# Optimization experiments

Hardware: AMD Instinct MI355X
Metric: run time of the kernel (lower is better)

The kernel has to match this reference:

```python
import jax, jax.numpy as jnp
import numpy as np

B, S, FEAT, H, DK, MAX_ITEMS = 8, 1024, 512, 8, 64, 200
LN_EPS = 1e-5
NEG = -999999999.0


def _build_mask(seq_len):
    # rows before T = S-(maxItems+1) cannot see the tail block [T:];
    # tail rows T..S-2 cannot see columns >= their own index (strict upper wedge).
    T = seq_len - (MAX_ITEMS + 1)
    i = jnp.arange(seq_len)[:, None]
    j = jnp.arange(seq_len)[None, :]
    blocked = ((i < T) & (j >= T)) | ((i >= T) & (i <= seq_len - 2) & (j >= i))
    return jnp.where(blocked, NEG, 0.0).astype(jnp.float32)  # [S, S]


def setup_inputs() -> dict:
    key = jax.random.key(0)
    ks = jax.random.split(key, 6)
    def init(k, shape, fan_in):
        return (jax.random.normal(k, shape, jnp.float32) / np.sqrt(fan_in)).astype(jnp.float32)
    return {
        "x": jax.random.normal(ks[0], (B, S, FEAT), jnp.float32),
        "ln_gamma": jnp.ones((FEAT,), jnp.float32),
        "ln_beta": jnp.zeros((FEAT,), jnp.float32),
        "WQ": init(ks[1], (H, FEAT, DK), FEAT), "bq": jnp.zeros((H, DK), jnp.float32),
        "WK": init(ks[2], (H, FEAT, DK), FEAT), "bk": jnp.zeros((H, DK), jnp.float32),
        "WV": init(ks[3], (H, FEAT, DK), FEAT), "bv": jnp.zeros((H, DK), jnp.float32),
        "WO": init(ks[4], (H * DK, FEAT), H * DK), "bO": jnp.zeros((FEAT,), jnp.float32),
    }


def reference(x, ln_gamma, ln_beta, WQ, bq, WK, bk, WV, bv, WO, bO):
    b, s, f = x.shape
    # Pre-LN
    mu = jnp.mean(x, axis=-1, keepdims=True)
    var = jnp.mean((x - mu) ** 2, axis=-1, keepdims=True)
    xn = (x - mu) / jnp.sqrt(var + LN_EPS) * ln_gamma + ln_beta
    # per-head projections, heads stacked: [B, H, S, DK]
    q = jnp.einsum('bsf,hfd->bhsd', xn, WQ) + bq[None, :, None, :]
    k = jnp.einsum('bsf,hfd->bhsd', xn, WK) + bk[None, :, None, :]
    v = jnp.einsum('bsf,hfd->bhsd', xn, WV) + bv[None, :, None, :]
    scores = jnp.einsum('bhsd,bhtd->bhst', q, k) / np.sqrt(DK).astype(np.float32)
    scores = scores + _build_mask(s)[None, None, :, :]
    attn = jax.nn.softmax(scores, axis=-1)
    z = jnp.einsum('bhst,bhtd->bhsd', attn, v)           # [B, H, S, DK]
    z = jnp.transpose(z, (0, 2, 1, 3)).reshape(b, s, -1)  # concat heads -> [B, S, H*DK]
    return z @ WO + bO
```

## Files before the change

kernel.cpp:

```cpp
#include <hip/hip_runtime.h>

typedef __bf16 bf16;
typedef __attribute__((ext_vector_type(8))) __bf16 bf16x8;
typedef __attribute__((ext_vector_type(4))) __bf16 bf16x4;
typedef __attribute__((ext_vector_type(4))) float f32x4;

#define QSCL 0.18033688011112042f
#define RESCALE_THR 8.0f

#if __has_builtin(__builtin_amdgcn_exp2f)
#define EXP2(x) __builtin_amdgcn_exp2f(x)
#else
#define EXP2(x) exp2f(x)
#endif

__device__ __forceinline__ void gload16(const void* g, void* l) {
  __builtin_amdgcn_global_load_lds(
      (const __attribute__((address_space(1))) void*)g,
      (__attribute__((address_space(3))) void*)l, 16, 0, 0);
}

__global__ void pack_kernel(const float* __restrict__ WQ, const float* __restrict__ WK,
                            const float* __restrict__ WV, const float* __restrict__ WO,
                            bf16* __restrict__ Bt, bf16* __restrict__ WOt) {
  int idx = blockIdx.x * 256 + threadIdx.x;
  if (idx < 1536 * 512) {
    int n = idx >> 9, k = idx & 511;
    int mat = n >> 9, rem = n & 511, h = rem >> 6, d = rem & 63;
    const float* W = (mat == 0) ? WQ : ((mat == 1) ? WK : WV);
    Bt[idx] = (bf16)W[((size_t)h * 512 + k) * 64 + d];
  } else {
    int j = idx - 1536 * 512;
    int n = j >> 9, k = j & 511;
    WOt[j] = (bf16)WO[(size_t)k * 512 + n];
  }
}

__global__ void ln_kernel(const float* __restrict__ x, const float* __restrict__ gam,
                          const float* __restrict__ bet, bf16* __restrict__ xn) {
  int wave = threadIdx.x >> 6, lane = threadIdx.x & 63;
  int row = blockIdx.x * 4 + wave;
  const float4* xr = (const float4*)(x + (size_t)row * 512);
  float4 v0 = xr[lane], v1 = xr[lane + 64];
  float s  = v0.x + v0.y + v0.z + v0.w + v1.x + v1.y + v1.z + v1.w;
  float s2 = v0.x * v0.x + v0.y * v0.y + v0.z * v0.z + v0.w * v0.w
           + v1.x * v1.x + v1.y * v1.y + v1.z * v1.z + v1.w * v1.w;
  #pragma unroll
  for (int m = 1; m < 64; m <<= 1) { s += __shfl_xor(s, m); s2 += __shfl_xor(s2, m); }
  float mu = s * (1.f / 512.f);
  float rstd = rsqrtf(s2 * (1.f / 512.f) - mu * mu + 1e-5f);
  const float4* gr = (const float4*)gam;
  const float4* br = (const float4*)bet;
  float4 g0 = gr[lane], g1 = gr[lane + 64], b0 = br[lane], b1 = br[lane + 64];
  bf16x4 o0, o1;
  o0[0] = (bf16)((v0.x - mu) * rstd * g0.x + b0.x);
  o0[1] = (bf16)((v0.y - mu) * rstd * g0.y + b0.y);
  o0[2] = (bf16)((v0.z - mu) * rstd * g0.z + b0.z);
  o0[3] = (bf16)((v0.w - mu) * rstd * g0.w + b0.w);
  o1[0] = (bf16)((v1.x - mu) * rstd * g1.x + b1.x);
  o1[1] = (bf16)((v1.y - mu) * rstd * g1.y + b1.y);
  o1[2] = (bf16)((v1.z - mu) * rstd * g1.z + b1.z);
  o1[3] = (bf16)((v1.w - mu) * rstd * g1.w + b1.w);
  *(bf16x4*)(xn + (size_t)row * 512 + lane * 4) = o0;
  *(bf16x4*)(xn + (size_t)row * 512 + 256 + lane * 4) = o1;
}

template <int MODE>
__global__ __launch_bounds__(256) void gemm_kernel(
    const bf16* __restrict__ A, const bf16* __restrict__ Bt, float* __restrict__ outF,
    bf16* __restrict__ qb, bf16* __restrict__ kb, bf16* __restrict__ vtb,
    const float* __restrict__ biasQ, const float* __restrict__ biasK,
    const float* __restrict__ biasV, const float* __restrict__ biasO) {
  __shared__ bf16 sA[128 * 32];
  __shared__ bf16 sB[128 * 32];
  const int tid = threadIdx.x;
  const int wave = tid >> 6, lane = tid & 63;
  const int m0 = blockIdx.x * 128, n0 = blockIdx.y * 128;
  const int wm = (wave >> 1) * 64, wn = (wave & 1) * 64;
  const int lrow = lane & 15, lk = (lane >> 4) * 8;
  const int srow = lane >> 2, scol = (lane & 3) * 8;
  f32x4 acc[4][4] = {};
  for (int kt = 0; kt < 512; kt += 32) {
    __syncthreads();
    #pragma unroll
    for (int c = 0; c < 2; ++c) {
      const int ch = wave * 2 + c;
      gload16(A + (size_t)(m0 + ch * 16 + srow) * 512 + kt + scol, &sA[ch * 512]);
      gload16(Bt + (size_t)(n0 + ch * 16 + srow) * 512 + kt + scol, &sB[ch * 512]);
    }
    __syncthreads();
    bf16x8 af[4], bfr[4];
    #pragma unroll
    for (int mi = 0; mi < 4; ++mi)
      af[mi] = *(const bf16x8*)&sA[(wm + mi * 16 + lrow) * 32 + lk];
    #pragma unroll
    for (int ni = 0; ni < 4; ++ni)
      bfr[ni] = *(const bf16x8*)&sB[(wn + ni * 16 + lrow) * 32 + lk];
    #pragma unroll
    for (int mi = 0; mi < 4; ++mi)
      #pragma unroll
      for (int ni = 0; ni < 4; ++ni)
        acc[mi][ni] = __builtin_amdgcn_mfma_f32_16x16x32_bf16(af[mi], bfr[ni], acc[mi][ni], 0, 0, 0);
  }
  if (MODE == 0) {
    #pragma unroll
    for (int ni = 0; ni < 4; ++ni) {
      const int n = n0 + wn + ni * 16 + lrow;
      const int mat = n >> 9, rem = n & 511;
      const int hh = rem >> 6, d = rem & 63;
      const float bias = (mat == 0 ? biasQ : (mat == 1 ? biasK : biasV))[rem];
      #pragma unroll
      for (int mi = 0; mi < 4; ++mi) {
        #pragma unroll
        for (int r = 0; r < 4; ++r) {
          const int m = m0 + wm + mi * 16 + (lane >> 4) * 4 + r;
          const int bb = m >> 10, ss = m & 1023;
          float val = acc[mi][ni][r] + bias;
          if (mat == 2)
            vtb[(((size_t)bb * 8 + hh) * 64 + d) * 1024 + ss] = (bf16)val;
          else if (mat == 1)
            kb[(((size_t)bb * 8 + hh) * 1024 + ss) * 64 + d] = (bf16)val;
          else
            qb[(((size_t)bb * 8 + hh) * 1024 + ss) * 64 + d] = (bf16)(val * QSCL);
        }
      }
    }
  } else {
    #pragma unroll
    for (int ni = 0; ni < 4; ++ni) {
      const int n = n0 + wn + ni * 16 + lrow;
      const float bias = biasO[n];
      #pragma unroll
      for (int mi = 0; mi < 4; ++mi) {
        #pragma unroll
        for (int r = 0; r < 4; ++r) {
          const int m = m0 + wm + mi * 16 + (lane >> 4) * 4 + r;
          outF[(size_t)m * 512 + n] = acc[mi][ni][r] + bias;
        }
      }
    }
  }
}

__global__ __launch_bounds__(256) void attn_kernel(
    const bf16* __restrict__ qbuf, const bf16* __restrict__ kbuf,
    const bf16* __restrict__ vtbuf, bf16* __restrict__ z) {
  __shared__ bf16 sK[2][4096];
  __shared__ bf16 sV[2][4096];
  __shared__ bf16 pshared[4][16][64];
  const int tid = threadIdx.x;
  const int wave = tid >> 6, lane = tid & 63;
  const int bh = blockIdx.x;
  const int b = bh >> 3, h = bh & 7;
  const int q0 = blockIdx.y * 64 + wave * 16;
  const int lrow = lane & 15, lg = lane >> 4;
  const bf16* Q  = qbuf  + (size_t)bh * 65536;
  const bf16* Kp = kbuf  + (size_t)bh * 65536;
  const bf16* Vt = vtbuf + (size_t)bh * 65536;
  int srow[2], scol[2];
  #pragma unroll
  for (int cc = 0; cc < 2; ++cc) {
    const int d = wave * 2048 + cc * 1024 + lane * 16;
    srow[cc] = d >> 7;
    scol[cc] = ((d & 127) ^ ((srow[cc] & 7) << 4)) >> 1;
  }
  bf16x8 aq0, aq1;
  {
    const bf16* qs = Q + (size_t)(q0 + lrow) * 64 + lg * 8;
    aq0 = *(const bf16x8*)qs;
    aq1 = *(const bf16x8*)(qs + 32);
  }
  bf16x8 ones;
  #pragma unroll
  for (int i = 0; i < 8; ++i) ones[i] = (bf16)1.0f;
  float mrow[4] = {-1e30f, -1e30f, -1e30f, -1e30f};
  float lsum[4] = {0.f, 0.f, 0.f, 0.f};
  f32x4 o[4] = {};
  const int qmax = blockIdx.y * 64 + 63;
  const int jend = (qmax >= 1023) ? 1024 : (qmax > 823 ? qmax : 823);
  const int ntile = (jend + 63) >> 6;
  #pragma unroll
  for (int cc = 0; cc < 2; ++cc) {
    const int dbase = wave * 2048 + cc * 1024;
    gload16(Kp + (size_t)srow[cc] * 64 + scol[cc], (char*)sK[0] + dbase);
    gload16(Vt + (size_t)srow[cc] * 1024 + scol[cc], (char*)sV[0] + dbase);
  }
  __syncthreads();
  for (int jt = 0; jt < ntile; ++jt) {
    const int j0 = jt * 64;
    const int cur = jt & 1;
    if (jt + 1 < ntile) {
      const int j1 = j0 + 64;
      #pragma unroll
      for (int cc = 0; cc < 2; ++cc) {
        const int dbase = wave * 2048 + cc * 1024;
        gload16(Kp + (size_t)(j1 + srow[cc]) * 64 + scol[cc], (char*)sK[cur ^ 1] + dbase);
        gload16(Vt + (size_t)srow[cc] * 1024 + j1 + scol[cc], (char*)sV[cur ^ 1] + dbase);
      }
    }
    f32x4 sc[4];
    __builtin_amdgcn_s_setprio(1);
    #pragma unroll
    for (int ct = 0; ct < 4; ++ct) {
      const int row = ct * 16 + lrow;
      const int sw = (row & 7) << 4;
      const bf16x8 kb0 = *(const bf16x8*)((char*)sK[cur] + row * 128 + ((lg * 16) ^ sw));
      const bf16x8 kb1 = *(const bf16x8*)((char*)sK[cur] + row * 128 + ((64 + lg * 16) ^ sw));
      f32x4 c = {0.f, 0.f, 0.f, 0.f};
      c = __builtin_amdgcn_mfma_f32_16x16x32_bf16(aq0, kb0, c, 0, 0, 0);
      c = __builtin_amdgcn_mfma_f32_16x16x32_bf16(aq1, kb1, c, 0, 0, 0);
      sc[ct] = c;
    }
    __builtin_amdgcn_s_setprio(0);
    if (jt == ntile - 1) {
      #pragma unroll
      for (int ct = 0; ct < 4; ++ct)
        #pragma unroll
        for (int r = 0; r < 4; ++r) {
          const int i = q0 + lg * 4 + r;
          const int j = j0 + ct * 16 + lrow;
          const bool blk = (i < 823 && j >= 823) || (i >= 823 && i <= 1022 && j >= i);
          if (blk) sc[ct][r] = -1e9f;
        }
    }
    float tmax[4];
    #pragma unroll
    for (int r = 0; r < 4; ++r)
      tmax[r] = fmaxf(fmaxf(sc[0][r], sc[1][r]), fmaxf(sc[2][r], sc[3][r]));
    #pragma unroll
    for (int r = 0; r < 4; ++r) {
      float v = tmax[r];
      v = fmaxf(v, __shfl_xor(v, 1, 16));
      v = fmaxf(v, __shfl_xor(v, 2, 16));
      v = fmaxf(v, __shfl_xor(v, 4, 16));
      v = fmaxf(v, __shfl_xor(v, 8, 16));
      tmax[r] = v;
    }
    const float g = fmaxf(fmaxf(tmax[0] - mrow[0], tmax[1] - mrow[1]),
                          fmaxf(tmax[2] - mrow[2], tmax[3] - mrow[3]));
    if (g > RESCALE_THR) {
      #pragma unroll
      for (int r = 0; r < 4; ++r) {
        const float mn = fmaxf(mrow[r], tmax[r]);
        const float corr = EXP2(mrow[r] - mn);
        mrow[r] = mn;
        lsum[r] *= corr;
        #pragma unroll
        for (int nt = 0; nt < 4; ++nt) o[nt][r] *= corr;
      }
    }
    #pragma unroll
    for (int ct = 0; ct < 4; ++ct)
      #pragma unroll
      for (int r = 0; r < 4; ++r) {
        const float p = EXP2(sc[ct][r] - mrow[r]);
        const int row = lg * 4 + r;
        pshared[wave][row][(ct * 16 + lrow) ^ ((row & 7) << 3)] = (bf16)p;
      }
    f32x4 ps = {0.f, 0.f, 0.f, 0.f};
    __builtin_amdgcn_s_setprio(1);
    #pragma unroll
    for (int kc = 0; kc < 2; ++kc) {
      const bf16x8 pa = *(const bf16x8*)&pshared[wave][lrow][(kc * 32 + lg * 8) ^ ((lrow & 7) << 3)];
      ps = __builtin_amdgcn_mfma_f32_16x16x32_bf16(pa, ones, ps, 0, 0, 0);
      #pragma unroll
      for (int nt = 0; nt < 4; ++nt) {
        const int row = nt * 16 + lrow;
        const int sw = (row & 7) << 4;
        const bf16x8 vb = *(const bf16x8*)((char*)sV[cur] + row * 128 + ((kc * 64 + lg * 16) ^ sw));
        o[nt] = __builtin_amdgcn_mfma_f32_16x16x32_bf16(pa, vb, o[nt], 0, 0, 0);
      }
    }
    __builtin_amdgcn_s_setprio(0);
    #pragma unroll
    for (int r = 0; r < 4; ++r) lsum[r] += ps[r];
    __syncthreads();
  }
  #pragma unroll
  for (int r = 0; r < 4; ++r) {
    const float inv = 1.f / lsum[r];
    #pragma unroll
    for (int nt = 0; nt < 4; ++nt) o[nt][r] *= inv;
  }
  #pragma unroll
  for (int nt = 0; nt < 4; ++nt)
    #pragma unroll
    for (int r = 0; r < 4; ++r) {
      const int ss = q0 + lg * 4 + r;
      z[((size_t)b * 1024 + ss) * 512 + h * 64 + nt * 16 + lrow] = (bf16)o[nt][r];
    }
}

extern "C" void kernel_launch(void* const* d_in, const int* in_sizes, int n_in,
                              void* d_out, int out_size, void* d_ws, size_t ws_size,
                              hipStream_t stream) {
  const float* x  = (const float*)d_in[0];
  const float* g  = (const float*)d_in[1];
  const float* be = (const float*)d_in[2];
  const float* WQ = (const float*)d_in[3];
  const float* bq = (const float*)d_in[4];
  const float* WK = (const float*)d_in[5];
  const float* bk = (const float*)d_in[6];
  const float* WV = (const float*)d_in[7];
  const float* bv = (const float*)d_in[8];
  const float* WO = (const float*)d_in[9];
  const float* bO = (const float*)d_in[10];
  float* out = (float*)d_out;
  char* ws = (char*)d_ws;
  bf16* xn  = (bf16*)(ws);
  bf16* Bt  = (bf16*)(ws + 8388608);
  bf16* WOt = (bf16*)(ws + 9961472);
  bf16* qb  = (bf16*)(ws + 10485760);
  bf16* kb  = (bf16*)(ws + 18874368);
  bf16* vtb = (bf16*)(ws + 27262976);
  pack_kernel<<<4096, 256, 0, stream>>>(WQ, WK, WV, WO, Bt, WOt);
  ln_kernel<<<2048, 256, 0, stream>>>(x, g, be, xn);
  gemm_kernel<0><<<dim3(64, 12), 256, 0, stream>>>(xn, Bt, nullptr, qb, kb, vtb, bq, bk, bv, nullptr);
  attn_kernel<<<dim3(64, 16), 256, 0, stream>>>(qb, kb, vtb, xn );
  gemm_kernel<1><<<dim3(64, 4), 256, 0, stream>>>(xn, WOt, out, nullptr, nullptr, nullptr,
                                                  nullptr, nullptr, nullptr, bO);
}
```

Before: 180.6 us.

## Rewrite attention with 32x32 MFMA register softmax, double-buffer GEMM, tiled weight pack

```diff
diff --git a/kernel.cpp b/kernel.cpp
--- a/kernel.cpp
+++ b/kernel.cpp
@@ -3,16 +3,12 @@
 typedef __bf16 bf16;
 typedef __attribute__((ext_vector_type(8))) __bf16 bf16x8;
 typedef __attribute__((ext_vector_type(4))) __bf16 bf16x4;
+typedef __attribute__((ext_vector_type(2))) __bf16 bf16x2;
 typedef __attribute__((ext_vector_type(4))) float f32x4;
+typedef __attribute__((ext_vector_type(16))) float f32x16;
 
 #define QSCL 0.18033688011112042f
 #define RESCALE_THR 8.0f
-
-#if __has_builtin(__builtin_amdgcn_exp2f)
-#define EXP2(x) __builtin_amdgcn_exp2f(x)
-#else
-#define EXP2(x) exp2f(x)
-#endif
 
 __device__ __forceinline__ void gload16(const void* g, void* l) {
   __builtin_amdgcn_global_load_lds(
@@ -20,19 +16,53 @@
       (__attribute__((address_space(3))) void*)l, 16, 0, 0);
 }
 
-__global__ void pack_kernel(const float* __restrict__ WQ, const float* __restrict__ WK,
-                            const float* __restrict__ WV, const float* __restrict__ WO,
-                            bf16* __restrict__ Bt, bf16* __restrict__ WOt) {
-  int idx = blockIdx.x * 256 + threadIdx.x;
-  if (idx < 1536 * 512) {
-    int n = idx >> 9, k = idx & 511;
-    int mat = n >> 9, rem = n & 511, h = rem >> 6, d = rem & 63;
+__device__ __forceinline__ unsigned pack2bf(float a, float b) {
+  union { bf16x2 v; unsigned u; } t;
+  t.v[0] = (bf16)a; t.v[1] = (bf16)b;
+  return t.u;
+}
+__device__ __forceinline__ float bperm_f(int byteaddr, float v) {
+  return __int_as_float(__builtin_amdgcn_ds_bpermute(byteaddr, __float_as_int(v)));
+}
+
+__global__ __launch_bounds__(256) void pack_kernel(
+    const float* __restrict__ WQ, const float* __restrict__ WK,
+    const float* __restrict__ WV, const float* __restrict__ WO,
+    bf16* __restrict__ Bt, bf16* __restrict__ WOt) {
+  __shared__ float t[32][33];
+  const int tid = threadIdx.x;
+  const int tx = tid & 31, ty = tid >> 5;
+  const int bid = blockIdx.x;
+  if (bid < 768) {
+    const int g = bid >> 5, rem = bid & 31;
+    const int db = rem >> 4, kb = rem & 15;
+    const int mat = g >> 3, h = g & 7;
     const float* W = (mat == 0) ? WQ : ((mat == 1) ? WK : WV);
-    Bt[idx] = (bf16)W[((size_t)h * 512 + k) * 64 + d];
+    #pragma unroll
+    for (int r = 0; r < 4; ++r) {
+      const int kloc = r * 8 + ty;
+      t[kloc][tx] = W[((size_t)h * 512 + kb * 32 + kloc) * 64 + db * 32 + tx];
+    }
+    __syncthreads();
+    #pragma unroll
+    for (int r = 0; r < 4; ++r) {
+      const int dloc = r * 8 + ty;
+      Bt[((size_t)mat * 512 + h * 64 + db * 32 + dloc) * 512 + kb * 32 + tx] = (bf16)t[tx][dloc];
+    }
   } else {
-    int j = idx - 1536 * 512;
-    int n = j >> 9, k = j & 511;
-    WOt[j] = (bf16)WO[(size_t)k * 512 + n];
+    const int bid2 = bid - 768;
+    const int nb = bid2 >> 4, kb = bid2 & 15;
+    #pragma unroll
+    for (int r = 0; r < 4; ++r) {
+      const int kloc = r * 8 + ty;
+      t[kloc][tx] = WO[((size_t)kb * 32 + kloc) * 512 + nb * 32 + tx];
+    }
+    __syncthreads();
+    #pragma unroll
+    for (int r = 0; r < 4; ++r) {
+      const int nloc = r * 8 + ty;
+      WOt[((size_t)nb * 32 + nloc) * 512 + kb * 32 + tx] = (bf16)t[tx][nloc];
+    }
   }
 }
 
@@ -71,8 +101,8 @@
     bf16* __restrict__ qb, bf16* __restrict__ kb, bf16* __restrict__ vtb,
     const float* __restrict__ biasQ, const float* __restrict__ biasK,
     const float* __restrict__ biasV, const float* __restrict__ biasO) {
-  __shared__ bf16 sA[128 * 32];
-  __shared__ bf16 sB[128 * 32];
+  __shared__ bf16 sA[2][128 * 32];
+  __shared__ bf16 sB[2][128 * 32];
   const int tid = threadIdx.x;
   const int wave = tid >> 6, lane = tid & 63;
   const int m0 = blockIdx.x * 128, n0 = blockIdx.y * 128;
@@ -80,27 +110,39 @@
   const int lrow = lane & 15, lk = (lane >> 4) * 8;
   const int srow = lane >> 2, scol = (lane & 3) * 8;
   f32x4 acc[4][4] = {};
+  #pragma unroll
+  for (int c = 0; c < 2; ++c) {
+    const int ch = wave * 2 + c;
+    gload16(A + (size_t)(m0 + ch * 16 + srow) * 512 + scol, &sA[0][ch * 512]);
+    gload16(Bt + (size_t)(n0 + ch * 16 + srow) * 512 + scol, &sB[0][ch * 512]);
+  }
+  __syncthreads();
+  int buf = 0;
   for (int kt = 0; kt < 512; kt += 32) {
-    __syncthreads();
-    #pragma unroll
-    for (int c = 0; c < 2; ++c) {
-      const int ch = wave * 2 + c;
-      gload16(A + (size_t)(m0 + ch * 16 + srow) * 512 + kt + scol, &sA[ch * 512]);
-      gload16(Bt + (size_t)(n0 + ch * 16 + srow) * 512 + kt + scol, &sB[ch * 512]);
-    }
-    __syncthreads();
+    if (kt + 32 < 512) {
+      #pragma unroll
+      for (int c = 0; c < 2; ++c) {
+        const int ch = wave * 2 + c;
+        gload16(A + (size_t)(m0 + ch * 16 + srow) * 512 + kt + 32 + scol, &sA[buf ^ 1][ch * 512]);
+        gload16(Bt + (size_t)(n0 + ch * 16 + srow) * 512 + kt + 32 + scol, &sB[buf ^ 1][ch * 512]);
+      }
+    }
     bf16x8 af[4], bfr[4];
     #pragma unroll
     for (int mi = 0; mi < 4; ++mi)
-      af[mi] = *(const bf16x8*)&sA[(wm + mi * 16 + lrow) * 32 + lk];
+      af[mi] = *(const bf16x8*)&sA[buf][(wm + mi * 16 + lrow) * 32 + lk];
     #pragma unroll
     for (int ni = 0; ni < 4; ++ni)
-      bfr[ni] = *(const bf16x8*)&sB[(wn + ni * 16 + lrow) * 32 + lk];
+      bfr[ni] = *(const bf16x8*)&sB[buf][(wn + ni * 16 + lrow) * 32 + lk];
+    __builtin_amdgcn_s_setprio(1);
     #pragma unroll
     for (int mi = 0; mi < 4; ++mi)
       #pragma unroll
       for (int ni = 0; ni < 4; ++ni)
         acc[mi][ni] = __builtin_amdgcn_mfma_f32_16x16x32_bf16(af[mi], bfr[ni], acc[mi][ni], 0, 0, 0);
+    __builtin_amdgcn_s_setprio(0);
+    __syncthreads();
+    buf ^= 1;
   }
   if (MODE == 0) {
     #pragma unroll
@@ -142,153 +184,153 @@
   }
 }
 
-__global__ __launch_bounds__(256) void attn_kernel(
+__global__ __launch_bounds__(256, 2) void attn_kernel(
     const bf16* __restrict__ qbuf, const bf16* __restrict__ kbuf,
     const bf16* __restrict__ vtbuf, bf16* __restrict__ z) {
-  __shared__ bf16 sK[2][4096];
-  __shared__ bf16 sV[2][4096];
-  __shared__ bf16 pshared[4][16][64];
+  __shared__ __align__(16) char sK[2][8192];
+  __shared__ __align__(16) char sV[2][8192];
   const int tid = threadIdx.x;
   const int wave = tid >> 6, lane = tid & 63;
   const int bh = blockIdx.x;
   const int b = bh >> 3, h = bh & 7;
-  const int q0 = blockIdx.y * 64 + wave * 16;
-  const int lrow = lane & 15, lg = lane >> 4;
+  const int y = blockIdx.y;
+  const int q0 = y * 128 + wave * 32;
+  const int ql = lane & 31, hf = lane >> 5;
   const bf16* Q  = qbuf  + (size_t)bh * 65536;
-  const bf16* Kp = kbuf  + (size_t)bh * 65536;
+  const bf16* K  = kbuf  + (size_t)bh * 65536;
   const bf16* Vt = vtbuf + (size_t)bh * 65536;
-  int srow[2], scol[2];
+
+  bf16x8 qf[4];
+  #pragma unroll
+  for (int s = 0; s < 4; ++s)
+    qf[s] = *(const bf16x8*)(Q + (size_t)(q0 + ql) * 64 + s * 16 + hf * 8);
+
+  int kOff[2], vOff[2], dstO[2];
   #pragma unroll
   for (int cc = 0; cc < 2; ++cc) {
-    const int d = wave * 2048 + cc * 1024 + lane * 16;
-    srow[cc] = d >> 7;
-    scol[cc] = ((d & 127) ^ ((srow[cc] & 7) << 4)) >> 1;
-  }
-  bf16x8 aq0, aq1;
-  {
-    const bf16* qs = Q + (size_t)(q0 + lrow) * 64 + lg * 8;
-    aq0 = *(const bf16x8*)qs;
-    aq1 = *(const bf16x8*)(qs + 32);
-  }
-  bf16x8 ones;
-  #pragma unroll
-  for (int i = 0; i < 8; ++i) ones[i] = (bf16)1.0f;
-  float mrow[4] = {-1e30f, -1e30f, -1e30f, -1e30f};
-  float lsum[4] = {0.f, 0.f, 0.f, 0.f};
-  f32x4 o[4] = {};
-  const int qmax = blockIdx.y * 64 + 63;
-  const int jend = (qmax >= 1023) ? 1024 : (qmax > 823 ? qmax : 823);
-  const int ntile = (jend + 63) >> 6;
+    const int p = wave * 1024 + cc * 4096 + lane * 16;
+    const int row = p >> 8, inner = p & 255;
+    const int inn = inner ^ ((row & 15) << 4);
+    const int src_row = row + (inn >> 7) * 32;
+    const int colb = inn & 127;
+    kOff[cc] = src_row * 128 + colb;
+    vOff[cc] = src_row * 2048 + colb;
+    dstO[cc] = wave * 1024 + cc * 4096;
+  }
+  const int hs = (hf * 16) ^ ((ql & 15) << 4);
+  const int rbase = ql * 256;
+  const int iq = q0 + ql;
+  const int thr = (iq < 823) ? 823 : ((iq == 1023) ? 1024 : iq);
+
+  float m = -1e30f, lsum = 0.f;
+  f32x16 og[2] = {};
+  const int ntile = (y == 7) ? 16 : ((y == 6) ? 14 : 13);
+
   #pragma unroll
   for (int cc = 0; cc < 2; ++cc) {
-    const int dbase = wave * 2048 + cc * 1024;
-    gload16(Kp + (size_t)srow[cc] * 64 + scol[cc], (char*)sK[0] + dbase);
-    gload16(Vt + (size_t)srow[cc] * 1024 + scol[cc], (char*)sV[0] + dbase);
+    gload16((const char*)K + kOff[cc], sK[0] + dstO[cc]);
+    gload16((const char*)Vt + vOff[cc], sV[0] + dstO[cc]);
   }
   __syncthreads();
+
   for (int jt = 0; jt < ntile; ++jt) {
     const int j0 = jt * 64;
     const int cur = jt & 1;
     if (jt + 1 < ntile) {
-      const int j1 = j0 + 64;
       #pragma unroll
       for (int cc = 0; cc < 2; ++cc) {
-        const int dbase = wave * 2048 + cc * 1024;
-        gload16(Kp + (size_t)(j1 + srow[cc]) * 64 + scol[cc], (char*)sK[cur ^ 1] + dbase);
-        gload16(Vt + (size_t)srow[cc] * 1024 + j1 + scol[cc], (char*)sV[cur ^ 1] + dbase);
-      }
-    }
-    f32x4 sc[4];
+        gload16((const char*)K + (size_t)(j0 + 64) * 128 + kOff[cc], sK[cur ^ 1] + dstO[cc]);
+        gload16((const char*)Vt + (size_t)(j0 + 64) * 2 + vOff[cc], sV[cur ^ 1] + dstO[cc]);
+      }
+    }
+    f32x16 st[2] = {};
     __builtin_amdgcn_s_setprio(1);
     #pragma unroll
-    for (int ct = 0; ct < 4; ++ct) {
-      const int row = ct * 16 + lrow;
-      const int sw = (row & 7) << 4;
-      const bf16x8 kb0 = *(const bf16x8*)((char*)sK[cur] + row * 128 + ((lg * 16) ^ sw));
-      const bf16x8 kb1 = *(const bf16x8*)((char*)sK[cur] + row * 128 + ((64 + lg * 16) ^ sw));
-      f32x4 c = {0.f, 0.f, 0.f, 0.f};
-      c = __builtin_amdgcn_mfma_f32_16x16x32_bf16(aq0, kb0, c, 0, 0, 0);
-      c = __builtin_amdgcn_mfma_f32_16x16x32_bf16(aq1, kb1, c, 0, 0, 0);
-      sc[ct] = c;
-    }
+    for (int bb = 0; bb < 2; ++bb)
+      #pragma unroll
+      for (int s = 0; s < 4; ++s) {
+        const bf16x8 kf = *(const bf16x8*)(sK[cur] + rbase + ((bb * 128 + s * 32) ^ hs));
+        st[bb] = __builtin_amdgcn_mfma_f32_32x32x16_bf16(kf, qf[s], st[bb], 0, 0, 0);
+      }
     __builtin_amdgcn_s_setprio(0);
-    if (jt == ntile - 1) {
-      #pragma unroll
-      for (int ct = 0; ct < 4; ++ct)
+    if (j0 + 63 >= 823) {
+      #pragma unroll
+      for (int bb = 0; bb < 2; ++bb)
         #pragma unroll
-        for (int r = 0; r < 4; ++r) {
-          const int i = q0 + lg * 4 + r;
-          const int j = j0 + ct * 16 + lrow;
-          const bool blk = (i < 823 && j >= 823) || (i >= 823 && i <= 1022 && j >= i);
-          if (blk) sc[ct][r] = -1e9f;
+        for (int rg = 0; rg < 16; ++rg) {
+          const int kv = j0 + bb * 32 + (rg & 3) + 8 * (rg >> 2) + 4 * hf;
+          if (kv >= thr) st[bb][rg] = -1e9f;
         }
     }
-    float tmax[4];
-    #pragma unroll
-    for (int r = 0; r < 4; ++r)
-      tmax[r] = fmaxf(fmaxf(sc[0][r], sc[1][r]), fmaxf(sc[2][r], sc[3][r]));
-    #pragma unroll
-    for (int r = 0; r < 4; ++r) {
-      float v = tmax[r];
-      v = fmaxf(v, __shfl_xor(v, 1, 16));
-      v = fmaxf(v, __shfl_xor(v, 2, 16));
-      v = fmaxf(v, __shfl_xor(v, 4, 16));
-      v = fmaxf(v, __shfl_xor(v, 8, 16));
-      tmax[r] = v;
-    }
-    const float g = fmaxf(fmaxf(tmax[0] - mrow[0], tmax[1] - mrow[1]),
-                          fmaxf(tmax[2] - mrow[2], tmax[3] - mrow[3]));
-    if (g > RESCALE_THR) {
-      #pragma unroll
-      for (int r = 0; r < 4; ++r) {
-        const float mn = fmaxf(mrow[r], tmax[r]);
-        const float corr = EXP2(mrow[r] - mn);
-        mrow[r] = mn;
-        lsum[r] *= corr;
+    float mx = st[0][0];
+    #pragma unroll
+    for (int rg = 1; rg < 16; ++rg) mx = fmaxf(mx, st[0][rg]);
+    #pragma unroll
+    for (int rg = 0; rg < 16; ++rg) mx = fmaxf(mx, st[1][rg]);
+    mx = fmaxf(mx, __shfl_xor(mx, 32));
+    if (__any(mx - m > RESCALE_THR)) {
+      const float pm = fmaxf(m, mx);
+      const float corr = exp2f(m - pm);
+      m = pm;
+      lsum *= corr;
+      #pragma unroll
+      for (int rg = 0; rg < 16; ++rg) {
+        const float oc = bperm_f((((rg & 3) + 8 * (rg >> 2) + 4 * hf) << 2), corr);
+        og[0][rg] *= oc;
+        og[1][rg] *= oc;
+      }
+    }
+    unsigned pk[2][8];
+    float ps = 0.f;
+    #pragma unroll
+    for (int bb = 0; bb < 2; ++bb)
+      #pragma unroll
+      for (int c = 0; c < 4; ++c) {
+        const float p0 = exp2f(st[bb][4 * c + 0] - m);
+        const float p1 = exp2f(st[bb][4 * c + 1] - m);
+        const float p2 = exp2f(st[bb][4 * c + 2] - m);
+        const float p3 = exp2f(st[bb][4 * c + 3] - m);
+        ps += (p0 + p1) + (p2 + p3);
+        pk[bb][c * 2 + 0] = pack2bf(p0, p1);
+        pk[bb][c * 2 + 1] = pack2bf(p2, p3);
+      }
+    lsum += ps;
+    unsigned sw[2][8];
+    #pragma unroll
+    for (int bb = 0; bb < 2; ++bb)
+      #pragma unroll
+      for (int w = 0; w < 8; ++w) sw[bb][w] = __shfl_xor(pk[bb][w], 32);
+    __builtin_amdgcn_s_setprio(1);
+    #pragma unroll
+    for (int bb = 0; bb < 2; ++bb)
+      #pragma unroll
+      for (int tt = 0; tt < 2; ++tt) {
+        union { unsigned u[4]; bf16x8 v; } fr;
+        fr.u[0] = hf ? sw[bb][(2 * tt + 1) * 2 + 0] : pk[bb][(2 * tt) * 2 + 0];
+        fr.u[1] = hf ? sw[bb][(2 * tt + 1) * 2 + 1] : pk[bb][(2 * tt) * 2 + 1];
+        fr.u[2] = hf ? pk[bb][(2 * tt + 1) * 2 + 0] : sw[bb][(2 * tt) * 2 + 0];
+        fr.u[3] = hf ? pk[bb][(2 * tt + 1) * 2 + 1] : sw[bb][(2 * tt) * 2 + 1];
+        const int step = bb * 2 + tt;
         #pragma unroll
-        for (int nt = 0; nt < 4; ++nt) o[nt][r] *= corr;
-      }
-    }
-    #pragma unroll
-    for (int ct = 0; ct < 4; ++ct)
-      #pragma unroll
-      for (int r = 0; r < 4; ++r) {
-        const float p = EXP2(sc[ct][r] - mrow[r]);
-        const int row = lg * 4 + r;
-        pshared[wave][row][(ct * 16 + lrow) ^ ((row & 7) << 3)] = (bf16)p;
-      }
-    f32x4 ps = {0.f, 0.f, 0.f, 0.f};
-    __builtin_amdgcn_s_setprio(1);
-    #pragma unroll
-    for (int kc = 0; kc < 2; ++kc) {
-      const bf16x8 pa = *(const bf16x8*)&pshared[wave][lrow][(kc * 32 + lg * 8) ^ ((lrow & 7) << 3)];
-      ps = __builtin_amdgcn_mfma_f32_16x16x32_bf16(pa, ones, ps, 0, 0, 0);
-      #pragma unroll
-      for (int nt = 0; nt < 4; ++nt) {
-        const int row = nt * 16 + lrow;
-        const int sw = (row & 7) << 4;
-        const bf16x8 vb = *(const bf16x8*)((char*)sV[cur] + row * 128 + ((kc * 64 + lg * 16) ^ sw));
-        o[nt] = __builtin_amdgcn_mfma_f32_16x16x32_bf16(pa, vb, o[nt], 0, 0, 0);
-      }
-    }
+        for (int g = 0; g < 2; ++g) {
+          const bf16x8 vf = *(const bf16x8*)(sV[cur] + rbase + ((g * 128 + step * 32) ^ hs));
+          og[g] = __builtin_amdgcn_mfma_f32_32x32x16_bf16(fr.v, vf, og[g], 0, 0, 0);
+        }
+      }
     __builtin_amdgcn_s_setprio(0);
-    #pragma unroll
-    for (int r = 0; r < 4; ++r) lsum[r] += ps[r];
     __syncthreads();
   }
-  #pragma unroll
-  for (int r = 0; r < 4; ++r) {
-    const float inv = 1.f / lsum[r];
-    #pragma unroll
-    for (int nt = 0; nt < 4; ++nt) o[nt][r] *= inv;
-  }
-  #pragma unroll
-  for (int nt = 0; nt < 4; ++nt)
-    #pragma unroll
-    for (int r = 0; r < 4; ++r) {
-      const int ss = q0 + lg * 4 + r;
-      z[((size_t)b * 1024 + ss) * 512 + h * 64 + nt * 16 + lrow] = (bf16)o[nt][r];
-    }
+  lsum += __shfl_xor(lsum, 32);
+  const float inv = 1.f / lsum;
+  #pragma unroll
+  for (int rg = 0; rg < 16; ++rg) {
+    const int rowq = (rg & 3) + 8 * (rg >> 2) + 4 * hf;
+    const float oinv = bperm_f(rowq << 2, inv);
+    const int q_abs = q0 + rowq;
+    #pragma unroll
+    for (int g = 0; g < 2; ++g)
+      z[((size_t)b * 1024 + q_abs) * 512 + h * 64 + g * 32 + ql] = (bf16)(og[g][rg] * oinv);
+  }
 }
 
 extern "C" void kernel_launch(void* const* d_in, const int* in_sizes, int n_in,
@@ -313,10 +355,10 @@
   bf16* qb  = (bf16*)(ws + 10485760);
   bf16* kb  = (bf16*)(ws + 18874368);
   bf16* vtb = (bf16*)(ws + 27262976);
-  pack_kernel<<<4096, 256, 0, stream>>>(WQ, WK, WV, WO, Bt, WOt);
+  pack_kernel<<<1024, 256, 0, stream>>>(WQ, WK, WV, WO, Bt, WOt);
   ln_kernel<<<2048, 256, 0, stream>>>(x, g, be, xn);
   gemm_kernel<0><<<dim3(64, 12), 256, 0, stream>>>(xn, Bt, nullptr, qb, kb, vtb, bq, bk, bv, nullptr);
-  attn_kernel<<<dim3(64, 16), 256, 0, stream>>>(qb, kb, vtb, xn );
+  attn_kernel<<<dim3(64, 8), 256, 0, stream>>>(qb, kb, vtb, xn );
   gemm_kernel<1><<<dim3(64, 4), 256, 0, stream>>>(xn, WOt, out, nullptr, nullptr, nullptr,
                                                   nullptr, nullptr, nullptr, bO);
 }
```

Result: faster. 163.6 us (-9.4%).
